# Kernel optimization log

Measured on AMD Instinct MI355X. Metric: run time of the kernel, lower is better.

Reference implementation:

```python
import jax, jax.numpy as jnp
import numpy as np

B, L, M, IS = 64, 20, 16, 1024  # batch, headers/example, tokens/header, feature dim
EPS = 1e-12


def setup_inputs() -> dict:
    key = jax.random.key(0)
    ks = jax.random.split(key, 10)
    total = B * L
    s = 1.0 / np.sqrt(IS)
    return {
        "ctx": jax.random.normal(ks[0], (B, IS), jnp.float32),
        "wemb_hpu": jax.random.normal(ks[1], (total, M, IS), jnp.float32),
        "l_hpu": jnp.full((total,), M, jnp.int32),
        "l_hs": jnp.full((B,), L, jnp.int32),
        "U_w": jax.random.uniform(ks[2], (IS, IS), jnp.float32, -s, s),
        "U_b": jnp.zeros((IS,), jnp.float32),
        "V_w": jax.random.uniform(ks[3], (IS, IS), jnp.float32, -s, s),
        "V_b": jnp.zeros((IS,), jnp.float32),
        "enc_w": jax.random.uniform(ks[4], (IS, 2 * IS), jnp.float32, -s, s),
        "enc_b": jnp.zeros((IS,), jnp.float32),
        "gamma": jnp.ones((IS,), jnp.float32),
        "beta": jnp.zeros((IS,), jnp.float32),
    }


def reference(ctx, wemb_hpu, l_hpu, l_hs, U_w, U_b, V_w, V_b, enc_w, enc_b, gamma, beta):
    total = wemb_hpu.shape[0]
    bS = ctx.shape[0]
    seg = jnp.repeat(jnp.arange(bS), total // bS)  # header-unit -> example id (constant l_hs)
    wenc_u = ctx @ U_w.T + U_b                      # [B, IS]
    wenc_v = wemb_hpu @ V_w.T + V_b                 # [T, M, IS]
    # per-header attention over its M tokens: sum over feature dim, softmax over tokens
    attn = jnp.einsum('ti,tmi->tm', wenc_u[seg], wenc_v)   # [T, M]
    p = jax.nn.softmax(attn, axis=1)
    pooled = jnp.einsum('tm,tmi->ti', p, wemb_hpu)          # [T, IS]
    cat = jnp.concatenate([pooled, ctx[seg]], axis=-1)      # [T, 2*IS]
    h = cat @ enc_w.T + enc_b                               # [T, IS]
    # scatter into padded [B, mL_hs, IS] (constant lengths -> exact reshape)
    wenc_hs = h.reshape(bS, total // bS, -1)
    # TF-style LayerNorm (eps inside sqrt)
    u = wenc_hs.mean(-1, keepdims=True)
    s2 = ((wenc_hs - u) ** 2).mean(-1, keepdims=True)
    x = (wenc_hs - u) / jnp.sqrt(s2 + EPS)
    return gamma * x + beta
```

## Files before the change

### kernel.cpp

```cpp
#include <hip/hip_runtime.h>
#include <hip/hip_cooperative_groups.h>
#include <math.h>

namespace cg = cooperative_groups;

#define TPB   256
#define CGRID 768
#define NCU   256

constexpr int ISZ = 1024;
constexpr int NB  = 64;
constexpr int NL  = 20;
constexpr int NM  = 16;
constexpr int NT  = NB * NL;

typedef __attribute__((ext_vector_type(8))) short  bf16x8;
typedef __attribute__((ext_vector_type(4))) float  f32x4;

struct Args {
    const float *ctx, *wemb, *U_w, *U_b, *V_w, *enc_w, *enc_b, *gamma, *beta;
    float *Upart, *uv, *cenc, *out;
    unsigned short *Vth, *Vtl, *encb, *pooledb;
};

__device__ __forceinline__ unsigned short f2bf(float x) {
    unsigned int u = __builtin_bit_cast(unsigned int, x);
    unsigned int r = (u + 0x7fff + ((u >> 16) & 1)) >> 16;
    return (unsigned short)r;
}
__device__ __forceinline__ float bf2f(unsigned short h) {
    unsigned int u = ((unsigned int)h) << 16;
    return __builtin_bit_cast(float, u);
}
__device__ __forceinline__ void split4(float4 v, ushort4& h, ushort4& l) {
    h.x = f2bf(v.x); l.x = f2bf(v.x - bf2f(h.x));
    h.y = f2bf(v.y); l.y = f2bf(v.y - bf2f(h.y));
    h.z = f2bf(v.z); l.z = f2bf(v.z - bf2f(h.z));
    h.w = f2bf(v.w); l.w = f2bf(v.w - bf2f(h.w));
}
__device__ __forceinline__ void gld_lds16(const void* g, void* l) {
    __builtin_amdgcn_global_load_lds(
        (const __attribute__((address_space(1))) unsigned int*)g,
        (__attribute__((address_space(3))) unsigned int*)l, 16, 0, 0);
}

__device__ __forceinline__ void stage_hl(const float* __restrict__ src, int ld,
                                         int kbeg, unsigned char* ldsH,
                                         unsigned char* ldsL, int tid)
{
    #pragma unroll
    for (int r = 0; r < 4; ++r) {
        int idx = r * 256 + tid;
        int row = idx >> 4, cg4 = (idx & 15) << 2;
        float4 v = *(const float4*)&src[(size_t)row * ld + kbeg + cg4];
        ushort4 h, l; split4(v, h, l);
        int boff = row * 128 + ((cg4 << 1) ^ ((row & 7) << 4));
        *(ushort4*)(ldsH + boff) = h;
        *(ushort4*)(ldsL + boff) = l;
    }
}
__device__ __forceinline__ void stage_h(const float* __restrict__ src, int ld,
                                        int kbeg, unsigned char* ldsH, int tid)
{
    #pragma unroll
    for (int r = 0; r < 4; ++r) {
        int idx = r * 256 + tid;
        int row = idx >> 4, cg4 = (idx & 15) << 2;
        float4 v = *(const float4*)&src[(size_t)row * ld + kbeg + cg4];
        ushort4 h = { f2bf(v.x), f2bf(v.y), f2bf(v.z), f2bf(v.w) };
        int boff = row * 128 + ((cg4 << 1) ^ ((row & 7) << 4));
        *(ushort4*)(ldsH + boff) = h;
    }
}
__device__ __forceinline__ void stage_A_uv(const float* __restrict__ Upart,
                                           const float* __restrict__ U_b,
                                           int kbeg, unsigned char* ldsH,
                                           unsigned char* ldsL, int tid)
{
    #pragma unroll
    for (int r = 0; r < 4; ++r) {
        int idx = r * 256 + tid;
        int row = idx >> 4, cg4 = (idx & 15) << 2;
        int k = kbeg + cg4;
        float4 v = *(const float4*)&U_b[k];
        #pragma unroll
        for (int s = 0; s < 8; ++s) {
            float4 u = *(const float4*)&Upart[(size_t)(s * 64 + row) * ISZ + k];
            v.x += u.x; v.y += u.y; v.z += u.z; v.w += u.w;
        }
        ushort4 h, l; split4(v, h, l);
        int boff = row * 128 + ((cg4 << 1) ^ ((row & 7) << 4));
        *(ushort4*)(ldsH + boff) = h;
        *(ushort4*)(ldsL + boff) = l;
    }
}

__device__ __forceinline__ void comp_hl(const unsigned char* lds, f32x4 acc[2][2], int tid)
{
    const int wid = tid >> 6, lane = tid & 63;
    const int ln = lane & 15, kb = lane >> 4;
    const int wr = wid >> 1, wc = wid & 1;
    #pragma unroll
    for (int ks = 0; ks < 2; ++ks) {
        const int cb = ks * 64 + kb * 16;
        bf16x8 ah[2], al[2], bh[2], bl[2];
        #pragma unroll
        for (int m = 0; m < 2; ++m) {
            int ra = wr * 32 + m * 16 + ln;
            int off = ra * 128 + (cb ^ ((ra & 7) << 4));
            ah[m] = *(const bf16x8*)(lds + off);
            al[m] = *(const bf16x8*)(lds + 8192 + off);
        }
        #pragma unroll
        for (int n = 0; n < 2; ++n) {
            int rb = wc * 32 + n * 16 + ln;
            int off = rb * 128 + (cb ^ ((rb & 7) << 4));
            bh[n] = *(const bf16x8*)(lds + 16384 + off);
            bl[n] = *(const bf16x8*)(lds + 24576 + off);
        }
        #pragma unroll
        for (int m = 0; m < 2; ++m)
            #pragma unroll
            for (int n = 0; n < 2; ++n) {
                acc[m][n] = __builtin_amdgcn_mfma_f32_16x16x32_bf16(ah[m], bh[n], acc[m][n], 0, 0, 0);
                acc[m][n] = __builtin_amdgcn_mfma_f32_16x16x32_bf16(ah[m], bl[n], acc[m][n], 0, 0, 0);
                acc[m][n] = __builtin_amdgcn_mfma_f32_16x16x32_bf16(al[m], bh[n], acc[m][n], 0, 0, 0);
            }
    }
}
__device__ __forceinline__ void comp_h(const unsigned char* lds, f32x4 acc[2][2], int tid)
{
    const int wid = tid >> 6, lane = tid & 63;
    const int ln = lane & 15, kb = lane >> 4;
    const int wr = wid >> 1, wc = wid & 1;
    #pragma unroll
    for (int ks = 0; ks < 2; ++ks) {
        const int cb = ks * 64 + kb * 16;
        bf16x8 ah[2], bh[2];
        #pragma unroll
        for (int m = 0; m < 2; ++m) {
            int ra = wr * 32 + m * 16 + ln;
            ah[m] = *(const bf16x8*)(lds + ra * 128 + (cb ^ ((ra & 7) << 4)));
        }
        #pragma unroll
        for (int n = 0; n < 2; ++n) {
            int rb = wc * 32 + n * 16 + ln;
            bh[n] = *(const bf16x8*)(lds + 16384 + rb * 128 + (cb ^ ((rb & 7) << 4)));
        }
        #pragma unroll
        for (int m = 0; m < 2; ++m)
            #pragma unroll
            for (int n = 0; n < 2; ++n)
                acc[m][n] = __builtin_amdgcn_mfma_f32_16x16x32_bf16(ah[m], bh[n], acc[m][n], 0, 0, 0);
    }
}

__device__ void p1_task(const Args& A, int task, int tid, unsigned char* smem)
{
    const int wid = tid >> 6, lane = tid & 63;
    const int wr = wid >> 1, wc = wid & 1;
    const int cl = lane & 15, rg = lane >> 4;

    if (task < 128) {
        int i4 = (task * TPB + tid) << 2;
        if (i4 < NB * ISZ) {
            float4 z = {0.f, 0.f, 0.f, 0.f};
            *(float4*)&A.uv[i4] = z;
        } else {
            *(float4*)&A.cenc[i4 - NB * ISZ] = *(const float4*)&A.enc_b[i4 & (ISZ - 1)];
        }
    } else if (task < 256) {
        const int id = task - 128;
        const int s = id >> 4, n0 = (id & 15) * 64;
        const int kbeg = s * 128;
        f32x4 acc[2][2] = {};
        for (int kt = 0; kt < 2; ++kt) {
            const int kk = kbeg + kt * 64;
            stage_hl(A.ctx, ISZ, kk, smem, smem + 8192, tid);
            stage_hl(A.U_w + (size_t)n0 * ISZ, ISZ, kk, smem + 16384, smem + 24576, tid);
            __syncthreads();
            comp_hl(smem, acc, tid);
            __syncthreads();
        }
        #pragma unroll
        for (int m = 0; m < 2; ++m)
            #pragma unroll
            for (int n = 0; n < 2; ++n) {
                int col = n0 + wc * 32 + n * 16 + cl;
                #pragma unroll
                for (int j = 0; j < 4; ++j) {
                    int row = wr * 32 + m * 16 + rg * 4 + j;
                    A.Upart[(size_t)(s * 64 + row) * ISZ + col] = acc[m][n][j];
                }
            }
    } else if (task < 512) {
        float (*t)[65] = (float(*)[65])smem;
        const int id = task - 256;
        const int r0 = (id >> 4) * 64, c0 = (id & 15) * 64;
        const int tr = tid >> 4, tc = (tid & 15) * 4;
        #pragma unroll
        for (int i = 0; i < 4; ++i) {
            float4 v = *(const float4*)&A.V_w[(size_t)(r0 + tr + 16 * i) * ISZ + c0 + tc];
            t[tr + 16 * i][tc + 0] = v.x; t[tr + 16 * i][tc + 1] = v.y;
            t[tr + 16 * i][tc + 2] = v.z; t[tr + 16 * i][tc + 3] = v.w;
        }
        __syncthreads();
        #pragma unroll
        for (int i = 0; i < 4; ++i) {
            int rr = tr + 16 * i;
            float4 v = { t[tc + 0][rr], t[tc + 1][rr], t[tc + 2][rr], t[tc + 3][rr] };
            ushort4 h, l; split4(v, h, l);
            *(ushort4*)&A.Vth[(size_t)(c0 + rr) * ISZ + r0 + tc] = h;
            *(ushort4*)&A.Vtl[(size_t)(c0 + rr) * ISZ + r0 + tc] = l;
        }
        __syncthreads();
    } else {
        const int id = task - 512;
        const int c = tid << 2;
        #pragma unroll
        for (int r = 0; r < 4; ++r) {
            int row = id * 4 + r;
            float4 v = *(const float4*)&A.enc_w[(size_t)row * 2048 + c];
            ushort4 o = { f2bf(v.x), f2bf(v.y), f2bf(v.z), f2bf(v.w) };
            *(ushort4*)&A.encb[(size_t)row * ISZ + c] = o;
        }
    }
}

__device__ void p2_task(const Args& A, int task, int tid, unsigned char* smem)
{
    const int wid = tid >> 6, lane = tid & 63;
    const int wr = wid >> 1, wc = wid & 1;
    const int cl = lane & 15, rg = lane >> 4;

    if (task < 128) {
        const int s = task >> 4, n0 = (task & 15) * 64;
        const int kbeg = s * 128;
        const int srow = lane >> 3, sbyte = (lane & 7) << 4;
        const int swz = sbyte ^ (srow << 4);
        f32x4 acc[2][2] = {};
        for (int kt = 0; kt < 2; ++kt) {
            const int kk = kbeg + kt * 64;
            const int kbyte = kk * 2;
            #pragma unroll
            for (int i = 0; i < 2; ++i) {
                int r = wid * 8 + i * 32 + srow;
                size_t gb = (size_t)(n0 + r) * 2048 + kbyte + swz;
                gld_lds16((const char*)A.Vth + gb, (void*)(smem + 16384 + wid * 1024 + i * 4096));
                gld_lds16((const char*)A.Vtl + gb, (void*)(smem + 24576 + wid * 1024 + i * 4096));
            }
            stage_A_uv(A.Upart, A.U_b, kk, smem, smem + 8192, tid);
            __syncthreads();
            comp_hl(smem, acc, tid);
            __syncthreads();
        }
        #pragma unroll
        for (int m = 0; m < 2; ++m)
            #pragma unroll
            for (int n = 0; n < 2; ++n) {
                int col = n0 + wc * 32 + n * 16 + cl;
                #pragma unroll
                for (int j = 0; j < 4; ++j) {
                    int row = wr * 32 + m * 16 + rg * 4 + j;
                    atomicAdd(&A.uv[(size_t)row * ISZ + col], acc[m][n][j]);
                }
            }
    } else {
        const int id = task - 128;
        const int s = id >> 4, n0 = (id & 15) * 64;
        const int kbeg = s * 128;
        f32x4 acc[2][2] = {};
        for (int kt = 0; kt < 2; ++kt) {
            const int kk = kbeg + kt * 64;
            stage_h(A.ctx, ISZ, kk, smem, tid);
            stage_h(A.enc_w + (size_t)n0 * 2048 + 1024, 2048, kk, smem + 16384, tid);
            __syncthreads();
            comp_h(smem, acc, tid);
            __syncthreads();
        }
        #pragma unroll
        for (int m = 0; m < 2; ++m)
            #pragma unroll
            for (int n = 0; n < 2; ++n) {
                int col = n0 + wc * 32 + n * 16 + cl;
                #pragma unroll
                for (int j = 0; j < 4; ++j) {
                    int row = wr * 32 + m * 16 + rg * 4 + j;
                    atomicAdd(&A.cenc[(size_t)row * ISZ + col], acc[m][n][j]);
                }
            }
    }
}

__device__ void p3_task(const Args& A, int t, int tid, unsigned char* smem)
{
    float (*red)[4] = (float(*)[4])smem;
    float* att = (float*)(smem + 256);
    const int b = t / NL;
    const int lane = tid & 63, wid = tid >> 6;

    const float* w = A.wemb + (size_t)t * NM * ISZ;
    const int j0 = tid << 2;
    float4 u4 = *(const float4*)&A.uv[(size_t)b * ISZ + j0];

    float4 wv[NM];
    float part[NM];
    #pragma unroll
    for (int m = 0; m < NM; ++m) {
        wv[m] = *(const float4*)&w[m * ISZ + j0];
        part[m] = wv[m].x * u4.x + wv[m].y * u4.y + wv[m].z * u4.z + wv[m].w * u4.w;
    }
    #pragma unroll
    for (int m = 0; m < NM; ++m) {
        float v = part[m];
        #pragma unroll
        for (int off = 32; off > 0; off >>= 1) v += __shfl_down(v, off, 64);
        if (lane == 0) red[m][wid] = v;
    }
    __syncthreads();
    if (tid < NM) att[tid] = red[tid][0] + red[tid][1] + red[tid][2] + red[tid][3];
    __syncthreads();

    float mx = att[0];
    #pragma unroll
    for (int m = 1; m < NM; ++m) mx = fmaxf(mx, att[m]);
    float p[NM], sm = 0.0f;
    #pragma unroll
    for (int m = 0; m < NM; ++m) { p[m] = __expf(att[m] - mx); sm += p[m]; }
    float inv = 1.0f / sm;

    float4 acc = {0.0f, 0.0f, 0.0f, 0.0f};
    #pragma unroll
    for (int m = 0; m < NM; ++m) {
        float pm = p[m] * inv;
        acc.x += pm * wv[m].x; acc.y += pm * wv[m].y;
        acc.z += pm * wv[m].z; acc.w += pm * wv[m].w;
    }
    ushort4 o;
    o.x = f2bf(acc.x); o.y = f2bf(acc.y); o.z = f2bf(acc.z); o.w = f2bf(acc.w);
    *(ushort4*)&A.pooledb[(size_t)t * ISZ + j0] = o;
    __syncthreads();
}

__device__ void p4_task(const Args& A, int task, int tid, unsigned char* smem)
{
    const int wid = tid >> 6, lane = tid & 63;
    const int wr = wid >> 1, wc = wid & 1;
    const int cl = lane & 15, rg = lane >> 4;
    const int m0 = (task >> 4) * 128;
    const int n0 = (task & 15) * 64;
    const int ln = lane & 15, kb = lane >> 4;
    const int srow = lane >> 3, sbyte = (lane & 7) << 4;
    const int swz = sbyte ^ (srow << 4);

    f32x4 acc[4][2] = {};
    const char* Abase = (const char*)A.pooledb;
    const char* Bbase = (const char*)A.encb;

    for (int kt = 0; kt < 16; ++kt) {
        const int kbyte = kt * 128;
        #pragma unroll
        for (int i = 0; i < 4; ++i) {
            int r = wid * 8 + i * 32 + srow;
            gld_lds16(Abase + ((size_t)(m0 + r) * ISZ) * 2 + kbyte + swz,
                      (void*)(smem + wid * 1024 + i * 4096));
        }
        #pragma unroll
        for (int i = 0; i < 2; ++i) {
            int r = wid * 8 + i * 32 + srow;
            gld_lds16(Bbase + ((size_t)(n0 + r) * ISZ) * 2 + kbyte + swz,
                      (void*)(smem + 16384 + wid * 1024 + i * 4096));
        }
        __syncthreads();
        #pragma unroll
        for (int ks = 0; ks < 2; ++ks) {
            const int cb = (ks * 64 + kb * 16);
            bf16x8 a[4], b[2];
            #pragma unroll
            for (int m = 0; m < 4; ++m) {
                int ra = wr * 64 + m * 16 + ln;
                a[m] = *(const bf16x8*)(smem + ra * 128 + (cb ^ ((ra & 7) << 4)));
            }
            #pragma unroll
            for (int n = 0; n < 2; ++n) {
                int rb = wc * 32 + n * 16 + ln;
                b[n] = *(const bf16x8*)(smem + 16384 + rb * 128 + (cb ^ ((rb & 7) << 4)));
            }
            #pragma unroll
            for (int m = 0; m < 4; ++m)
                #pragma unroll
                for (int n = 0; n < 2; ++n)
                    acc[m][n] = __builtin_amdgcn_mfma_f32_16x16x32_bf16(a[m], b[n], acc[m][n], 0, 0, 0);
        }
        __syncthreads();
    }
    #pragma unroll
    for (int m = 0; m < 4; ++m) {
        #pragma unroll
        for (int n = 0; n < 2; ++n) {
            int col = n0 + wc * 32 + n * 16 + cl;
            #pragma unroll
            for (int j = 0; j < 4; ++j) {
                int row = m0 + wr * 64 + m * 16 + rg * 4 + j;
                A.out[(size_t)row * ISZ + col] = acc[m][n][j] + A.cenc[(size_t)(row / NL) * ISZ + col];
            }
        }
    }
}

__device__ void p5_task(const Args& A, int t, int tid, unsigned char* smem)
{
    float* rs  = (float*)smem;
    float* rs2 = (float*)(smem + 16);
    float* mus = (float*)(smem + 32);
    const int lane = tid & 63, wid = tid >> 6;
    const int c = tid << 2;

    float4 v = *(const float4*)&A.out[(size_t)t * ISZ + c];
    float s  = v.x + v.y + v.z + v.w;
    float s2 = v.x * v.x + v.y * v.y + v.z * v.z + v.w * v.w;
    #pragma unroll
    for (int off = 32; off > 0; off >>= 1) {
        s  += __shfl_down(s, off, 64);
        s2 += __shfl_down(s2, off, 64);
    }
    if (lane == 0) { rs[wid] = s; rs2[wid] = s2; }
    __syncthreads();
    if (tid == 0) {
        float S  = rs[0] + rs[1] + rs[2] + rs[3];
        float S2 = rs2[0] + rs2[1] + rs2[2] + rs2[3];
        float m  = S / ISZ;
        float var = S2 / ISZ - m * m;
        mus[0] = m;
        mus[1] = rsqrtf(var + 1e-12f);
    }
    __syncthreads();
    const float mu = mus[0], rstd = mus[1];
    float4 g  = *(const float4*)&A.gamma[c];
    float4 be = *(const float4*)&A.beta[c];
    float4 o;
    o.x = g.x * (v.x - mu) * rstd + be.x;
    o.y = g.y * (v.y - mu) * rstd + be.y;
    o.z = g.z * (v.z - mu) * rstd + be.z;
    o.w = g.w * (v.w - mu) * rstd + be.w;
    *(float4*)&A.out[(size_t)t * ISZ + c] = o;
    __syncthreads();
}

__global__ __launch_bounds__(TPB, 4)
void fused_all(Args A)
{
    cg::grid_group grid = cg::this_grid();
    __shared__ __align__(16) unsigned char smem[32768];
    const int tid = threadIdx.x;

    for (int t = blockIdx.x; t < 768; t += gridDim.x) p1_task(A, t, tid, smem);
    grid.sync();
    for (int t = blockIdx.x; t < 256; t += gridDim.x) p2_task(A, t, tid, smem);
    grid.sync();
    for (int t = blockIdx.x; t < NT;  t += gridDim.x) p3_task(A, t, tid, smem);
    grid.sync();
    for (int t = blockIdx.x; t < 160; t += gridDim.x) p4_task(A, t, tid, smem);
    grid.sync();
    for (int t = blockIdx.x; t < NT;  t += gridDim.x) p5_task(A, t, tid, smem);
}

__global__ __launch_bounds__(TPB) void k_p1(Args A) {
    __shared__ __align__(16) unsigned char smem[32768];
    p1_task(A, blockIdx.x, threadIdx.x, smem);
}
__global__ __launch_bounds__(TPB) void k_p2(Args A) {
    __shared__ __align__(16) unsigned char smem[32768];
    p2_task(A, blockIdx.x, threadIdx.x, smem);
}
__global__ __launch_bounds__(TPB) void k_p3(Args A) {
    __shared__ __align__(16) unsigned char smem[512];
    p3_task(A, blockIdx.x, threadIdx.x, smem);
}
__global__ __launch_bounds__(TPB) void k_p4(Args A) {
    __shared__ __align__(16) unsigned char smem[24576];
    p4_task(A, blockIdx.x, threadIdx.x, smem);
}
__global__ __launch_bounds__(TPB) void k_p5(Args A) {
    __shared__ __align__(16) unsigned char smem[512];
    p5_task(A, blockIdx.x, threadIdx.x, smem);
}

extern "C" void kernel_launch(void* const* d_in, const int* in_sizes, int n_in,
                              void* d_out, int out_size, void* d_ws, size_t ws_size,
                              hipStream_t stream)
{
    Args A;
    A.ctx   = (const float*)d_in[0];
    A.wemb  = (const float*)d_in[1];
    A.U_w   = (const float*)d_in[4];
    A.U_b   = (const float*)d_in[5];
    A.V_w   = (const float*)d_in[6];
    A.enc_w = (const float*)d_in[8];
    A.enc_b = (const float*)d_in[9];
    A.gamma = (const float*)d_in[10];
    A.beta  = (const float*)d_in[11];
    A.out   = (float*)d_out;

    float* ws = (float*)d_ws;
    A.Upart = ws;
    A.uv    = ws + 8 * NB * ISZ;
    A.cenc  = A.uv + NB * ISZ;
    unsigned short* p = (unsigned short*)(A.cenc + NB * ISZ);
    A.Vth     = p;  p += ISZ * ISZ;
    A.Vtl     = p;  p += ISZ * ISZ;
    A.encb    = p;  p += ISZ * ISZ;
    A.pooledb = p;

    int nb = 0;
    hipError_t qe = hipOccupancyMaxActiveBlocksPerMultiprocessor(&nb, fused_all, TPB, 0);
    if (qe == hipSuccess && nb * NCU >= CGRID) {
        void* kargs[] = { (void*)&A };
        hipLaunchCooperativeKernel((const void*)fused_all, dim3(CGRID), dim3(TPB),
                                   kargs, 0, stream);
    } else {
        k_p1<<<768, TPB, 0, stream>>>(A);
        k_p2<<<256, TPB, 0, stream>>>(A);
        k_p3<<<NT,  TPB, 0, stream>>>(A);
        k_p4<<<160, TPB, 0, stream>>>(A);
        k_p5<<<NT,  TPB, 0, stream>>>(A);
    }
}
```

Measured before the change: 64.34 us.

## Replace cooperative grid syncs with flag-chained kernels and double-buffered encoder GEMM

The cooperative persistent kernel with four grid-wide barriers is replaced by four ordinary kernel launches preceded by a memset. In the first kernel, the dependent uv GEMM blocks now spin on atomic counters until the U partials and the V transposes finish, instead of waiting at a grid barrier. The encoder GEMM moves to smaller 64x64 tiles (320 blocks) with double-buffered async LDS loads, and enc_b is added in its epilogue. The spin-wait relies on the producer blocks being scheduled before or alongside the waiting blocks, so there is a deadlock risk if the hardware does not dispatch blocks in index order. The extra launches and the memset add fixed overhead.

```diff
diff --git a/kernel.cpp b/kernel.cpp
--- a/kernel.cpp
+++ b/kernel.cpp
@@ -1,12 +1,7 @@
 #include <hip/hip_runtime.h>
-#include <hip/hip_cooperative_groups.h>
 #include <math.h>
 
-namespace cg = cooperative_groups;
-
-#define TPB   256
-#define CGRID 768
-#define NCU   256
+#define TPB 256
 
 constexpr int ISZ = 1024;
 constexpr int NB  = 64;
@@ -19,7 +14,8 @@
 
 struct Args {
     const float *ctx, *wemb, *U_w, *U_b, *V_w, *enc_w, *enc_b, *gamma, *beta;
-    float *Upart, *uv, *cenc, *out;
+    float *uv, *cenc, *Upart, *out;
+    unsigned *flags;
     unsigned short *Vth, *Vtl, *encb, *pooledb;
 };
 
@@ -155,23 +151,17 @@
     }
 }
 
-__device__ void p1_task(const Args& A, int task, int tid, unsigned char* smem)
-{
+__global__ __launch_bounds__(TPB)
+void k_chain(Args A)
+{
+    __shared__ __align__(16) unsigned char smem[32768];
+    const int bid = blockIdx.x, tid = threadIdx.x;
     const int wid = tid >> 6, lane = tid & 63;
     const int wr = wid >> 1, wc = wid & 1;
     const int cl = lane & 15, rg = lane >> 4;
 
-    if (task < 128) {
-        int i4 = (task * TPB + tid) << 2;
-        if (i4 < NB * ISZ) {
-            float4 z = {0.f, 0.f, 0.f, 0.f};
-            *(float4*)&A.uv[i4] = z;
-        } else {
-            *(float4*)&A.cenc[i4 - NB * ISZ] = *(const float4*)&A.enc_b[i4 & (ISZ - 1)];
-        }
-    } else if (task < 256) {
-        const int id = task - 128;
-        const int s = id >> 4, n0 = (id & 15) * 64;
+    if (bid < 128) {
+        const int s = bid >> 4, n0 = (bid & 15) * 64;
         const int kbeg = s * 128;
         f32x4 acc[2][2] = {};
         for (int kt = 0; kt < 2; ++kt) {
@@ -193,80 +183,12 @@
                     A.Upart[(size_t)(s * 64 + row) * ISZ + col] = acc[m][n][j];
                 }
             }
-    } else if (task < 512) {
-        float (*t)[65] = (float(*)[65])smem;
-        const int id = task - 256;
-        const int r0 = (id >> 4) * 64, c0 = (id & 15) * 64;
-        const int tr = tid >> 4, tc = (tid & 15) * 4;
-        #pragma unroll
-        for (int i = 0; i < 4; ++i) {
-            float4 v = *(const float4*)&A.V_w[(size_t)(r0 + tr + 16 * i) * ISZ + c0 + tc];
-            t[tr + 16 * i][tc + 0] = v.x; t[tr + 16 * i][tc + 1] = v.y;
-            t[tr + 16 * i][tc + 2] = v.z; t[tr + 16 * i][tc + 3] = v.w;
-        }
+        __threadfence();
         __syncthreads();
-        #pragma unroll
-        for (int i = 0; i < 4; ++i) {
-            int rr = tr + 16 * i;
-            float4 v = { t[tc + 0][rr], t[tc + 1][rr], t[tc + 2][rr], t[tc + 3][rr] };
-            ushort4 h, l; split4(v, h, l);
-            *(ushort4*)&A.Vth[(size_t)(c0 + rr) * ISZ + r0 + tc] = h;
-            *(ushort4*)&A.Vtl[(size_t)(c0 + rr) * ISZ + r0 + tc] = l;
-        }
-        __syncthreads();
-    } else {
-        const int id = task - 512;
-        const int c = tid << 2;
-        #pragma unroll
-        for (int r = 0; r < 4; ++r) {
-            int row = id * 4 + r;
-            float4 v = *(const float4*)&A.enc_w[(size_t)row * 2048 + c];
-            ushort4 o = { f2bf(v.x), f2bf(v.y), f2bf(v.z), f2bf(v.w) };
-            *(ushort4*)&A.encb[(size_t)row * ISZ + c] = o;
-        }
-    }
-}
-
-__device__ void p2_task(const Args& A, int task, int tid, unsigned char* smem)
-{
-    const int wid = tid >> 6, lane = tid & 63;
-    const int wr = wid >> 1, wc = wid & 1;
-    const int cl = lane & 15, rg = lane >> 4;
-
-    if (task < 128) {
-        const int s = task >> 4, n0 = (task & 15) * 64;
-        const int kbeg = s * 128;
-        const int srow = lane >> 3, sbyte = (lane & 7) << 4;
-        const int swz = sbyte ^ (srow << 4);
-        f32x4 acc[2][2] = {};
-        for (int kt = 0; kt < 2; ++kt) {
-            const int kk = kbeg + kt * 64;
-            const int kbyte = kk * 2;
-            #pragma unroll
-            for (int i = 0; i < 2; ++i) {
-                int r = wid * 8 + i * 32 + srow;
-                size_t gb = (size_t)(n0 + r) * 2048 + kbyte + swz;
-                gld_lds16((const char*)A.Vth + gb, (void*)(smem + 16384 + wid * 1024 + i * 4096));
-                gld_lds16((const char*)A.Vtl + gb, (void*)(smem + 24576 + wid * 1024 + i * 4096));
-            }
-            stage_A_uv(A.Upart, A.U_b, kk, smem, smem + 8192, tid);
-            __syncthreads();
-            comp_hl(smem, acc, tid);
-            __syncthreads();
-        }
-        #pragma unroll
-        for (int m = 0; m < 2; ++m)
-            #pragma unroll
-            for (int n = 0; n < 2; ++n) {
-                int col = n0 + wc * 32 + n * 16 + cl;
-                #pragma unroll
-                for (int j = 0; j < 4; ++j) {
-                    int row = wr * 32 + m * 16 + rg * 4 + j;
-                    atomicAdd(&A.uv[(size_t)row * ISZ + col], acc[m][n][j]);
-                }
-            }
-    } else {
-        const int id = task - 128;
+        if (tid == 0)
+            __hip_atomic_fetch_add(&A.flags[0], 1u, __ATOMIC_RELEASE, __HIP_MEMORY_SCOPE_AGENT);
+    } else if (bid < 256) {
+        const int id = bid - 128;
         const int s = id >> 4, n0 = (id & 15) * 64;
         const int kbeg = s * 128;
         f32x4 acc[2][2] = {};
@@ -289,14 +211,92 @@
                     atomicAdd(&A.cenc[(size_t)row * ISZ + col], acc[m][n][j]);
                 }
             }
-    }
-}
-
-__device__ void p3_task(const Args& A, int t, int tid, unsigned char* smem)
-{
-    float (*red)[4] = (float(*)[4])smem;
-    float* att = (float*)(smem + 256);
+    } else if (bid < 512) {
+        float (*t)[65] = (float(*)[65])smem;
+        const int id = bid - 256;
+        const int r0 = (id >> 4) * 64, c0 = (id & 15) * 64;
+        const int tr = tid >> 4, tc = (tid & 15) * 4;
+        #pragma unroll
+        for (int i = 0; i < 4; ++i) {
+            float4 v = *(const float4*)&A.V_w[(size_t)(r0 + tr + 16 * i) * ISZ + c0 + tc];
+            t[tr + 16 * i][tc + 0] = v.x; t[tr + 16 * i][tc + 1] = v.y;
+            t[tr + 16 * i][tc + 2] = v.z; t[tr + 16 * i][tc + 3] = v.w;
+        }
+        __syncthreads();
+        #pragma unroll
+        for (int i = 0; i < 4; ++i) {
+            int rr = tr + 16 * i;
+            float4 v = { t[tc + 0][rr], t[tc + 1][rr], t[tc + 2][rr], t[tc + 3][rr] };
+            ushort4 h, l; split4(v, h, l);
+            *(ushort4*)&A.Vth[(size_t)(c0 + rr) * ISZ + r0 + tc] = h;
+            *(ushort4*)&A.Vtl[(size_t)(c0 + rr) * ISZ + r0 + tc] = l;
+        }
+        __threadfence();
+        __syncthreads();
+        if (tid == 0)
+            __hip_atomic_fetch_add(&A.flags[1], 1u, __ATOMIC_RELEASE, __HIP_MEMORY_SCOPE_AGENT);
+    } else if (bid < 640) {
+        const int id = bid - 512;
+        const int c = tid << 2;
+        #pragma unroll
+        for (int r = 0; r < 8; ++r) {
+            int row = id * 8 + r;
+            float4 v = *(const float4*)&A.enc_w[(size_t)row * 2048 + c];
+            ushort4 o = { f2bf(v.x), f2bf(v.y), f2bf(v.z), f2bf(v.w) };
+            *(ushort4*)&A.encb[(size_t)row * ISZ + c] = o;
+        }
+    } else {
+        if (tid == 0) {
+            while (__hip_atomic_load(&A.flags[0], __ATOMIC_RELAXED, __HIP_MEMORY_SCOPE_AGENT) < 128u ||
+                   __hip_atomic_load(&A.flags[1], __ATOMIC_RELAXED, __HIP_MEMORY_SCOPE_AGENT) < 256u)
+                __builtin_amdgcn_s_sleep(2);
+        }
+        __syncthreads();
+        __threadfence();
+
+        const int id = bid - 640;
+        const int s = id >> 4, n0 = (id & 15) * 64;
+        const int kbeg = s * 128;
+        const int srow = lane >> 3, sbyte = (lane & 7) << 4;
+        const int swz = sbyte ^ (srow << 4);
+        f32x4 acc[2][2] = {};
+        for (int kt = 0; kt < 2; ++kt) {
+            const int kk = kbeg + kt * 64;
+            const int kbyte = kk * 2;
+            #pragma unroll
+            for (int i = 0; i < 2; ++i) {
+                int r = wid * 8 + i * 32 + srow;
+                size_t gb = (size_t)(n0 + r) * 2048 + kbyte + swz;
+                gld_lds16((const char*)A.Vth + gb, (void*)(smem + 16384 + wid * 1024 + i * 4096));
+                gld_lds16((const char*)A.Vtl + gb, (void*)(smem + 24576 + wid * 1024 + i * 4096));
+            }
+            stage_A_uv(A.Upart, A.U_b, kk, smem, smem + 8192, tid);
+            __syncthreads();
+            comp_hl(smem, acc, tid);
+            __syncthreads();
+        }
+        #pragma unroll
+        for (int m = 0; m < 2; ++m)
+            #pragma unroll
+            for (int n = 0; n < 2; ++n) {
+                int col = n0 + wc * 32 + n * 16 + cl;
+                #pragma unroll
+                for (int j = 0; j < 4; ++j) {
+                    int row = wr * 32 + m * 16 + rg * 4 + j;
+                    atomicAdd(&A.uv[(size_t)row * ISZ + col], acc[m][n][j]);
+                }
+            }
+    }
+}
+
+__global__ __launch_bounds__(TPB)
+void k_attn(Args A)
+{
+    __shared__ float red[16][4];
+    __shared__ float att[16];
+    const int t = blockIdx.x;
     const int b = t / NL;
+    const int tid = threadIdx.x;
     const int lane = tid & 63, wid = tid >> 6;
 
     const float* w = A.wemb + (size_t)t * NM * ISZ;
@@ -339,80 +339,97 @@
     ushort4 o;
     o.x = f2bf(acc.x); o.y = f2bf(acc.y); o.z = f2bf(acc.z); o.w = f2bf(acc.w);
     *(ushort4*)&A.pooledb[(size_t)t * ISZ + j0] = o;
-    __syncthreads();
-}
-
-__device__ void p4_task(const Args& A, int task, int tid, unsigned char* smem)
-{
-    const int wid = tid >> 6, lane = tid & 63;
+}
+
+__global__ __launch_bounds__(TPB)
+void k_enc(Args A)
+{
+    __shared__ __align__(16) unsigned char smem[32768];
+    const int tid = threadIdx.x, wid = tid >> 6, lane = tid & 63;
+    const int m0 = (blockIdx.x >> 4) * 64;
+    const int n0 = (blockIdx.x & 15) * 64;
+    const int srow = lane >> 3;
+    const int swz  = ((lane & 7) << 4) ^ (srow << 4);
+    const char* Ab = (const char*)A.pooledb;
+    const char* Bb = (const char*)A.encb;
+
+#define STAGE_ENC(kt, buf) do {                                                  \
+        const int kbyte_ = (kt) * 128;                                           \
+        _Pragma("unroll")                                                        \
+        for (int i_ = 0; i_ < 2; ++i_) {                                         \
+            int r_ = wid * 8 + i_ * 32 + srow;                                   \
+            gld_lds16(Ab + ((size_t)(m0 + r_) * ISZ) * 2 + kbyte_ + swz,         \
+                      (void*)(smem + (buf) * 8192 + wid * 1024 + i_ * 4096));    \
+            gld_lds16(Bb + ((size_t)(n0 + r_) * ISZ) * 2 + kbyte_ + swz,         \
+                      (void*)(smem + 16384 + (buf) * 8192 + wid * 1024 + i_ * 4096)); \
+        } } while (0)
+
+    f32x4 acc[2][2] = {};
+    STAGE_ENC(0, 0);
+    STAGE_ENC(1, 1);
+
+    const int ln = lane & 15, kb = lane >> 4;
     const int wr = wid >> 1, wc = wid & 1;
-    const int cl = lane & 15, rg = lane >> 4;
-    const int m0 = (task >> 4) * 128;
-    const int n0 = (task & 15) * 64;
-    const int ln = lane & 15, kb = lane >> 4;
-    const int srow = lane >> 3, sbyte = (lane & 7) << 4;
-    const int swz = sbyte ^ (srow << 4);
-
-    f32x4 acc[4][2] = {};
-    const char* Abase = (const char*)A.pooledb;
-    const char* Bbase = (const char*)A.encb;
 
     for (int kt = 0; kt < 16; ++kt) {
-        const int kbyte = kt * 128;
-        #pragma unroll
-        for (int i = 0; i < 4; ++i) {
-            int r = wid * 8 + i * 32 + srow;
-            gld_lds16(Abase + ((size_t)(m0 + r) * ISZ) * 2 + kbyte + swz,
-                      (void*)(smem + wid * 1024 + i * 4096));
-        }
-        #pragma unroll
-        for (int i = 0; i < 2; ++i) {
-            int r = wid * 8 + i * 32 + srow;
-            gld_lds16(Bbase + ((size_t)(n0 + r) * ISZ) * 2 + kbyte + swz,
-                      (void*)(smem + 16384 + wid * 1024 + i * 4096));
-        }
-        __syncthreads();
+        const int cur = kt & 1;
+        if (kt < 15) asm volatile("s_waitcnt vmcnt(4)" ::: "memory");
+        else         asm volatile("s_waitcnt vmcnt(0)" ::: "memory");
+        __builtin_amdgcn_sched_barrier(0);
+        __builtin_amdgcn_s_barrier();
+        __builtin_amdgcn_sched_barrier(0);
+
         #pragma unroll
         for (int ks = 0; ks < 2; ++ks) {
-            const int cb = (ks * 64 + kb * 16);
-            bf16x8 a[4], b[2];
-            #pragma unroll
-            for (int m = 0; m < 4; ++m) {
-                int ra = wr * 64 + m * 16 + ln;
-                a[m] = *(const bf16x8*)(smem + ra * 128 + (cb ^ ((ra & 7) << 4)));
+            const int cb = ks * 64 + kb * 16;
+            bf16x8 a[2], b[2];
+            #pragma unroll
+            for (int m = 0; m < 2; ++m) {
+                int ra = wr * 32 + m * 16 + ln;
+                a[m] = *(const bf16x8*)(smem + cur * 8192 + ra * 128 + (cb ^ ((ra & 7) << 4)));
             }
             #pragma unroll
             for (int n = 0; n < 2; ++n) {
                 int rb = wc * 32 + n * 16 + ln;
-                b[n] = *(const bf16x8*)(smem + 16384 + rb * 128 + (cb ^ ((rb & 7) << 4)));
-            }
-            #pragma unroll
-            for (int m = 0; m < 4; ++m)
+                b[n] = *(const bf16x8*)(smem + 16384 + cur * 8192 + rb * 128 + (cb ^ ((rb & 7) << 4)));
+            }
+            #pragma unroll
+            for (int m = 0; m < 2; ++m)
                 #pragma unroll
                 for (int n = 0; n < 2; ++n)
                     acc[m][n] = __builtin_amdgcn_mfma_f32_16x16x32_bf16(a[m], b[n], acc[m][n], 0, 0, 0);
         }
-        __syncthreads();
-    }
-    #pragma unroll
-    for (int m = 0; m < 4; ++m) {
+
+        asm volatile("s_waitcnt lgkmcnt(0)" ::: "memory");
+        __builtin_amdgcn_sched_barrier(0);
+        __builtin_amdgcn_s_barrier();
+        __builtin_amdgcn_sched_barrier(0);
+        if (kt < 14) STAGE_ENC(kt + 2, cur);
+    }
+#undef STAGE_ENC
+
+    const int cl = lane & 15, rg = lane >> 4;
+    #pragma unroll
+    for (int m = 0; m < 2; ++m)
         #pragma unroll
         for (int n = 0; n < 2; ++n) {
             int col = n0 + wc * 32 + n * 16 + cl;
             #pragma unroll
             for (int j = 0; j < 4; ++j) {
-                int row = m0 + wr * 64 + m * 16 + rg * 4 + j;
-                A.out[(size_t)row * ISZ + col] = acc[m][n][j] + A.cenc[(size_t)(row / NL) * ISZ + col];
-            }
-        }
-    }
-}
-
-__device__ void p5_task(const Args& A, int t, int tid, unsigned char* smem)
-{
-    float* rs  = (float*)smem;
-    float* rs2 = (float*)(smem + 16);
-    float* mus = (float*)(smem + 32);
+                int row = m0 + wr * 32 + m * 16 + rg * 4 + j;
+                A.out[(size_t)row * ISZ + col] =
+                    acc[m][n][j] + A.cenc[(size_t)(row / NL) * ISZ + col] + A.enc_b[col];
+            }
+        }
+}
+
+__global__ __launch_bounds__(TPB)
+void k_ln(Args A)
+{
+    __shared__ float rs[4], rs2[4];
+    __shared__ float mu_s, rstd_s;
+    const int t = blockIdx.x;
+    const int tid = threadIdx.x;
     const int lane = tid & 63, wid = tid >> 6;
     const int c = tid << 2;
 
@@ -431,11 +448,11 @@
         float S2 = rs2[0] + rs2[1] + rs2[2] + rs2[3];
         float m  = S / ISZ;
         float var = S2 / ISZ - m * m;
-        mus[0] = m;
-        mus[1] = rsqrtf(var + 1e-12f);
+        mu_s  = m;
+        rstd_s = rsqrtf(var + 1e-12f);
     }
     __syncthreads();
-    const float mu = mus[0], rstd = mus[1];
+    const float mu = mu_s, rstd = rstd_s;
     float4 g  = *(const float4*)&A.gamma[c];
     float4 be = *(const float4*)&A.beta[c];
     float4 o;
@@ -444,46 +461,6 @@
     o.z = g.z * (v.z - mu) * rstd + be.z;
     o.w = g.w * (v.w - mu) * rstd + be.w;
     *(float4*)&A.out[(size_t)t * ISZ + c] = o;
-    __syncthreads();
-}
-
-__global__ __launch_bounds__(TPB, 4)
-void fused_all(Args A)
-{
-    cg::grid_group grid = cg::this_grid();
-    __shared__ __align__(16) unsigned char smem[32768];
-    const int tid = threadIdx.x;
-
-    for (int t = blockIdx.x; t < 768; t += gridDim.x) p1_task(A, t, tid, smem);
-    grid.sync();
-    for (int t = blockIdx.x; t < 256; t += gridDim.x) p2_task(A, t, tid, smem);
-    grid.sync();
-    for (int t = blockIdx.x; t < NT;  t += gridDim.x) p3_task(A, t, tid, smem);
-    grid.sync();
-    for (int t = blockIdx.x; t < 160; t += gridDim.x) p4_task(A, t, tid, smem);
-    grid.sync();
-    for (int t = blockIdx.x; t < NT;  t += gridDim.x) p5_task(A, t, tid, smem);
-}
-
-__global__ __launch_bounds__(TPB) void k_p1(Args A) {
-    __shared__ __align__(16) unsigned char smem[32768];
-    p1_task(A, blockIdx.x, threadIdx.x, smem);
-}
-__global__ __launch_bounds__(TPB) void k_p2(Args A) {
-    __shared__ __align__(16) unsigned char smem[32768];
-    p2_task(A, blockIdx.x, threadIdx.x, smem);
-}
-__global__ __launch_bounds__(TPB) void k_p3(Args A) {
-    __shared__ __align__(16) unsigned char smem[512];
-    p3_task(A, blockIdx.x, threadIdx.x, smem);
-}
-__global__ __launch_bounds__(TPB) void k_p4(Args A) {
-    __shared__ __align__(16) unsigned char smem[24576];
-    p4_task(A, blockIdx.x, threadIdx.x, smem);
-}
-__global__ __launch_bounds__(TPB) void k_p5(Args A) {
-    __shared__ __align__(16) unsigned char smem[512];
-    p5_task(A, blockIdx.x, threadIdx.x, smem);
 }
 
 extern "C" void kernel_launch(void* const* d_in, const int* in_sizes, int n_in,
@@ -503,26 +480,21 @@
     A.out   = (float*)d_out;
 
     float* ws = (float*)d_ws;
-    A.Upart = ws;
-    A.uv    = ws + 8 * NB * ISZ;
-    A.cenc  = A.uv + NB * ISZ;
-    unsigned short* p = (unsigned short*)(A.cenc + NB * ISZ);
+    A.uv    = ws;
+    A.cenc  = ws + NB * ISZ;
+    A.flags = (unsigned*)(ws + 2 * NB * ISZ);
+    A.Upart = (float*)(A.flags + 64);
+    unsigned short* p = (unsigned short*)(A.Upart + 8 * NB * ISZ);
     A.Vth     = p;  p += ISZ * ISZ;
     A.Vtl     = p;  p += ISZ * ISZ;
     A.encb    = p;  p += ISZ * ISZ;
     A.pooledb = p;
 
-    int nb = 0;
-    hipError_t qe = hipOccupancyMaxActiveBlocksPerMultiprocessor(&nb, fused_all, TPB, 0);
-    if (qe == hipSuccess && nb * NCU >= CGRID) {
-        void* kargs[] = { (void*)&A };
-        hipLaunchCooperativeKernel((const void*)fused_all, dim3(CGRID), dim3(TPB),
-                                   kargs, 0, stream);
-    } else {
-        k_p1<<<768, TPB, 0, stream>>>(A);
-        k_p2<<<256, TPB, 0, stream>>>(A);
-        k_p3<<<NT,  TPB, 0, stream>>>(A);
-        k_p4<<<160, TPB, 0, stream>>>(A);
-        k_p5<<<NT,  TPB, 0, stream>>>(A);
-    }
-}
+    hipMemsetAsync(A.uv, 0, (size_t)(2 * NB * ISZ) * sizeof(float) + 64 * sizeof(unsigned),
+                   stream);
+
+    k_chain<<<768, TPB, 0, stream>>>(A);
+    k_attn <<<NT,  TPB, 0, stream>>>(A);
+    k_enc  <<<320, TPB, 0, stream>>>(A);
+    k_ln   <<<NT,  TPB, 0, stream>>>(A);
+}
```

Measured after the change: 143.4 us. 123% more time.
